# Kernel tuning notes

Measured on AMD Instinct MI355X. Metric: run time of the kernel, lower is better.

Reference implementation:

```python
import jax, jax.numpy as jnp
import numpy as np

N = 100000   # nodes
E = 1600000  # edges
D = 64       # in_features == out_features (residual requires equality)
BN_EPS = 1e-5


def setup_inputs() -> dict:
    key = jax.random.key(0)
    ks = jax.random.split(key, 12)
    s = 1.0 / np.sqrt(D)
    inp = {
        "x": jax.random.normal(ks[0], (N, D), dtype=jnp.float32),
        "edge_index": jax.random.randint(ks[1], (2, E), 0, N, dtype=jnp.int64),
        # ResGatedGraphConv params: key/query/value/skip linears
        "Wk": jax.random.uniform(ks[2], (D, D), jnp.float32, -s, s),
        "bk": jax.random.uniform(ks[3], (D,), jnp.float32, -s, s),
        "Wq": jax.random.uniform(ks[4], (D, D), jnp.float32, -s, s),
        "bq": jax.random.uniform(ks[5], (D,), jnp.float32, -s, s),
        "Wv": jax.random.uniform(ks[6], (D, D), jnp.float32, -s, s),
        "bv": jax.random.uniform(ks[7], (D,), jnp.float32, -s, s),
        "Ws": jax.random.uniform(ks[8], (D, D), jnp.float32, -s, s),
        "bs": jax.random.uniform(ks[9], (D,), jnp.float32, -s, s),
        # BatchNorm1d affine params
        "gamma": jnp.ones((D,), jnp.float32),
        "beta": jnp.zeros((D,), jnp.float32),
    }
    return inp


def reference(x, edge_index, Wk, bk, Wq, bq, Wv, bv, Ws, bs, gamma, beta):
    # PyG ResGatedGraphConv:
    #   out_i = W_s x_i + b_s + sum_{(j->i)} sigmoid(k_i + q_j) * v_j
    # where k = lin_key(x), q = lin_query(x), v = lin_value(x).
    src = edge_index[0]  # source nodes j
    dst = edge_index[1]  # target nodes i

    k = x @ Wk.T + bk  # [N, D]
    q = x @ Wq.T + bq  # [N, D]
    v = x @ Wv.T + bv  # [N, D]

    gate = jax.nn.sigmoid(k[dst] + q[src])        # [E, D]
    msg = gate * v[src]                            # [E, D]
    agg = jax.ops.segment_sum(msg, dst, num_segments=x.shape[0])  # [N, D]

    h = agg + x @ Ws.T + bs

    # BatchNorm1d (training mode: batch statistics, biased variance)
    mean = jnp.mean(h, axis=0)
    var = jnp.var(h, axis=0)
    h = (h - mean) * jax.lax.rsqrt(var + BN_EPS) * gamma + beta

    h = jax.nn.relu(h)
    h = h + x  # residual
    # dropout: identity in eval / deterministic reference
    return h
```

## Files before the change

### kernel.cpp

```cpp
#include <hip/hip_runtime.h>
#include <hip/hip_bf16.h>
#include <math.h>

#define N_NODES 100000
#define N_EDGES 1600000
#define D_FEAT  64
#define BN_EPS  1e-5f

#define NBUCKET 196
#define NBUCKET_PAD 256
#define BUCKET_SHIFT 9
#define NBLK_E  196
#define EPB     8192
#define CCAP    96
#define DCAP    14336
#define GEMM_BLOCKS 1563

typedef __attribute__((ext_vector_type(8))) short bf16x8;
typedef __attribute__((ext_vector_type(4))) float f32x4;

static __device__ __forceinline__ short f2bf(float f) {
    __hip_bfloat16 h = __float2bfloat16(f);
    return __builtin_bit_cast(short, h);
}


__global__ __launch_bounds__(256) void gemm4_scatter_kernel(
    const float* __restrict__ x,
    const float* __restrict__ Wk, const float* __restrict__ bk,
    const float* __restrict__ Wq, const float* __restrict__ bq,
    const float* __restrict__ Wv, const float* __restrict__ bv,
    const float* __restrict__ Ws, const float* __restrict__ bs,
    unsigned char* __restrict__ mix,
    unsigned short* __restrict__ kp,
    float* __restrict__ h0,
    const int* __restrict__ ei,
    int* __restrict__ counts,
    unsigned int* __restrict__ chunks)
{
    __shared__ short xs[64 * 64];
    __shared__ unsigned short kt[64][68];
    __shared__ unsigned short qt[64][68];
    __shared__ unsigned short vt[64][68];
    __shared__ int hcnt[NBUCKET_PAD];

    if (blockIdx.x >= GEMM_BLOCKS) {
        const int cb = blockIdx.x - GEMM_BLOCKS;
        hcnt[threadIdx.x] = 0;
        __syncthreads();
        const int base = cb * EPB;
        for (int i = threadIdx.x; i < EPB; i += 256) {
            const int e = base + i;
            if (e < N_EDGES) {
                const int s = ei[e];
                const int d = ei[N_EDGES + e];
                const int b = d >> BUCKET_SHIFT;
                const int pos = atomicAdd(&hcnt[b], 1);
                if (pos < CCAP)
                    chunks[((size_t)b * NBLK_E + cb) * CCAP + pos] =
                        ((unsigned int)s << BUCKET_SHIFT) | (unsigned int)(d & 511);
            }
        }
        __syncthreads();
        if (threadIdx.x < NBUCKET)
            counts[threadIdx.x * NBLK_E + cb] = min(hcnt[threadIdx.x], CCAP);
        return;
    }

    const int lane = threadIdx.x & 63;
    const int wave = threadIdx.x >> 6;
    const int r0 = blockIdx.x * 64;

    const float* W; const float* b;
    if      (wave == 0) { W = Wk; b = bk; }
    else if (wave == 1) { W = Wq; b = bq; }
    else if (wave == 2) { W = Wv; b = bv; }
    else                { W = Ws; b = bs; }

    const int bcol = lane & 15;
    const int bk0  = (lane >> 4) * 8;
    bf16x8 bfrag[4][2];
    #pragma unroll
    for (int nt = 0; nt < 4; ++nt) {
        #pragma unroll
        for (int ks = 0; ks < 2; ++ks) {
            const float* wp = W + (nt * 16 + bcol) * 64 + ks * 32 + bk0;
            const float4 w0 = *reinterpret_cast<const float4*>(wp);
            const float4 w1 = *reinterpret_cast<const float4*>(wp + 4);
            bf16x8 f;
            f[0] = f2bf(w0.x); f[1] = f2bf(w0.y); f[2] = f2bf(w0.z); f[3] = f2bf(w0.w);
            f[4] = f2bf(w1.x); f[5] = f2bf(w1.y); f[6] = f2bf(w1.z); f[7] = f2bf(w1.w);
            bfrag[nt][ks] = f;
        }
    }
    float biasv[4];
    #pragma unroll
    for (int nt = 0; nt < 4; ++nt) biasv[nt] = b[nt * 16 + bcol];

    {
        const int row = threadIdx.x >> 2;
        const int qd  = threadIdx.x & 3;
        const int grow = r0 + row;
        float4 t0, t1, t2, t3;
        if (grow < N_NODES) {
            const float* xp = x + (size_t)grow * 64 + qd * 16;
            t0 = reinterpret_cast<const float4*>(xp)[0];
            t1 = reinterpret_cast<const float4*>(xp)[1];
            t2 = reinterpret_cast<const float4*>(xp)[2];
            t3 = reinterpret_cast<const float4*>(xp)[3];
        } else {
            t0 = t1 = t2 = t3 = make_float4(0.f, 0.f, 0.f, 0.f);
        }
        bf16x8 u0, u1;
        u0[0] = f2bf(t0.x); u0[1] = f2bf(t0.y); u0[2] = f2bf(t0.z); u0[3] = f2bf(t0.w);
        u0[4] = f2bf(t1.x); u0[5] = f2bf(t1.y); u0[6] = f2bf(t1.z); u0[7] = f2bf(t1.w);
        u1[0] = f2bf(t2.x); u1[1] = f2bf(t2.y); u1[2] = f2bf(t2.z); u1[3] = f2bf(t2.w);
        u1[4] = f2bf(t3.x); u1[5] = f2bf(t3.y); u1[6] = f2bf(t3.z); u1[7] = f2bf(t3.w);
        const int sw = row & 7;
        *reinterpret_cast<bf16x8*>(xs + row * 64 + (((qd * 2)     ^ sw) * 8)) = u0;
        *reinterpret_cast<bf16x8*>(xs + row * 64 + (((qd * 2 + 1) ^ sw) * 8)) = u1;
    }
    __syncthreads();

    f32x4 acc[4][4];
    #pragma unroll
    for (int mt = 0; mt < 4; ++mt)
        #pragma unroll
        for (int nt = 0; nt < 4; ++nt)
            acc[mt][nt] = (f32x4){biasv[nt], biasv[nt], biasv[nt], biasv[nt]};

    const int arow = lane & 15;
    const int ak   = lane >> 4;
    #pragma unroll
    for (int mt = 0; mt < 4; ++mt) {
        const int row = mt * 16 + arow;
        const int sw = row & 7;
        const bf16x8 a0 = *reinterpret_cast<const bf16x8*>(xs + row * 64 + ((ak       ^ sw) * 8));
        const bf16x8 a1 = *reinterpret_cast<const bf16x8*>(xs + row * 64 + (((4 + ak) ^ sw) * 8));
        #pragma unroll
        for (int nt = 0; nt < 4; ++nt) {
            acc[mt][nt] = __builtin_amdgcn_mfma_f32_16x16x32_bf16(
                a0, bfrag[nt][0], acc[mt][nt], 0, 0, 0);
            acc[mt][nt] = __builtin_amdgcn_mfma_f32_16x16x32_bf16(
                a1, bfrag[nt][1], acc[mt][nt], 0, 0, 0);
        }
    }

    const int crow0 = (lane >> 4) * 4;
    const int ccol  = lane & 15;
    if (wave < 3) {
        unsigned short (*tile)[68] = (wave == 0) ? kt : (wave == 1) ? qt : vt;
        #pragma unroll
        for (int mt = 0; mt < 4; ++mt)
            #pragma unroll
            for (int nt = 0; nt < 4; ++nt)
                #pragma unroll
                for (int r = 0; r < 4; ++r)
                    tile[mt * 16 + crow0 + r][nt * 16 + ccol] =
                        (unsigned short)f2bf(acc[mt][nt][r]);
    } else {
        #pragma unroll
        for (int mt = 0; mt < 4; ++mt)
            #pragma unroll
            for (int nt = 0; nt < 4; ++nt)
                #pragma unroll
                for (int r = 0; r < 4; ++r) {
                    const int grow = r0 + mt * 16 + crow0 + r;
                    if (grow < N_NODES)
                        h0[(size_t)grow * 64 + nt * 16 + ccol] = acc[mt][nt][r];
                }
    }
    __syncthreads();

    {
        const int row = threadIdx.x >> 2;
        const int seg = threadIdx.x & 3;
        const int grow = r0 + row;
        if (grow < N_NODES) {
            const int c0 = seg * 16;
            unsigned char* mrow = mix + (size_t)grow * 192;

            unsigned int qd[4];
            #pragma unroll
            for (int i = 0; i < 4; ++i) {
                const float f0 = __uint_as_float((unsigned int)qt[row][c0 + 4*i + 0] << 16);
                const float f1 = __uint_as_float((unsigned int)qt[row][c0 + 4*i + 1] << 16);
                const float f2 = __uint_as_float((unsigned int)qt[row][c0 + 4*i + 2] << 16);
                const float f3 = __uint_as_float((unsigned int)qt[row][c0 + 4*i + 3] << 16);
                int p = __builtin_amdgcn_cvt_pk_fp8_f32(f0, f1, 0, false);
                p = __builtin_amdgcn_cvt_pk_fp8_f32(f2, f3, p, true);
                qd[i] = (unsigned int)p;
            }
            *reinterpret_cast<uint4*>(mrow + c0) =
                make_uint4(qd[0], qd[1], qd[2], qd[3]);

            unsigned int vd[8];
            #pragma unroll
            for (int i = 0; i < 8; ++i)
                vd[i] = (unsigned int)vt[row][c0 + 2 * i] |
                        ((unsigned int)vt[row][c0 + 2 * i + 1] << 16);
            uint4* vdst = reinterpret_cast<uint4*>(mrow + 64 + seg * 32);
            vdst[0] = make_uint4(vd[0], vd[1], vd[2], vd[3]);
            vdst[1] = make_uint4(vd[4], vd[5], vd[6], vd[7]);

            unsigned int kd[8];
            #pragma unroll
            for (int i = 0; i < 8; ++i)
                kd[i] = (unsigned int)kt[row][c0 + 2 * i] |
                        ((unsigned int)kt[row][c0 + 2 * i + 1] << 16);
            uint4* kdst = reinterpret_cast<uint4*>(kp + (size_t)grow * 64 + c0);
            kdst[0] = make_uint4(kd[0], kd[1], kd[2], kd[3]);
            kdst[1] = make_uint4(kd[4], kd[5], kd[6], kd[7]);
        }
    }
}

__global__ __launch_bounds__(512) void bucket_sort_kernel(
    const int* __restrict__ counts,
    unsigned int* __restrict__ chunks,
    int2* __restrict__ row_se)
{
    __shared__ unsigned int stage[DCAP];
    __shared__ int hist[512];
    __shared__ int cursor[512];
    __shared__ int cpre[256];
    const int b = blockIdx.x;
    const int t = threadIdx.x;

    int myc = 0;
    if (t < 256) {
        myc = (t < NBLK_E) ? counts[b * NBLK_E + t] : 0;
        cpre[t] = myc;
    }
    __syncthreads();
    for (int off = 1; off < 256; off <<= 1) {
        int val = 0;
        if (t < 256 && t >= off) val = cpre[t - off];
        __syncthreads();
        if (t < 256) cpre[t] += val;
        __syncthreads();
    }
    const int total = cpre[255];

    if (t < NBLK_E && myc > 0) {
        const int dst0 = cpre[t] - myc;
        const unsigned int* src = chunks + ((size_t)b * NBLK_E + t) * CCAP;
        for (int c = 0; c < myc; ++c) {
            const int d = dst0 + c;
            if (d < DCAP) stage[d] = src[c];
        }
    }
    hist[t] = 0;
    __syncthreads();

    int sz = total;
    if (sz > DCAP) sz = DCAP;
    for (int i = t; i < sz; i += 512) atomicAdd(&hist[stage[i] & 511], 1);
    __syncthreads();
    const int myv = hist[t];
    for (int off = 1; off < 512; off <<= 1) {
        const int u = (t >= off) ? hist[t - off] : 0;
        __syncthreads();
        hist[t] += u;
        __syncthreads();
    }
    const int excl = hist[t] - myv;
    const int node = b * 512 + t;
    const int obase = b * NBLK_E * CCAP;
    if (node < N_NODES)
        row_se[node] = make_int2(obase + excl, obase + excl + myv);
    cursor[t] = excl;
    __syncthreads();

    unsigned int* out = chunks + (size_t)obase;
    for (int i = t; i < sz; i += 512) {
        const unsigned int pk = stage[i];
        const int pos = atomicAdd(&cursor[(int)(pk & 511)], 1);
        out[pos] = pk >> BUCKET_SHIFT;
    }
}

static __device__ __forceinline__ void edge4(
    float4& acc, const float4& kf, unsigned int qb, uint2 vb)
{
    const float q0 = __builtin_amdgcn_cvt_f32_fp8(qb, 0);
    const float q1 = __builtin_amdgcn_cvt_f32_fp8(qb, 1);
    const float q2 = __builtin_amdgcn_cvt_f32_fp8(qb, 2);
    const float q3 = __builtin_amdgcn_cvt_f32_fp8(qb, 3);
    const float v0 = __uint_as_float(vb.x << 16);
    const float v1 = __uint_as_float(vb.x & 0xffff0000u);
    const float v2 = __uint_as_float(vb.y << 16);
    const float v3 = __uint_as_float(vb.y & 0xffff0000u);
    acc.x = fmaf(__builtin_amdgcn_rcpf(1.0f + __expf(-(kf.x + q0))), v0, acc.x);
    acc.y = fmaf(__builtin_amdgcn_rcpf(1.0f + __expf(-(kf.y + q1))), v1, acc.y);
    acc.z = fmaf(__builtin_amdgcn_rcpf(1.0f + __expf(-(kf.z + q2))), v2, acc.z);
    acc.w = fmaf(__builtin_amdgcn_rcpf(1.0f + __expf(-(kf.w + q3))), v3, acc.w);
}

__global__ __launch_bounds__(256, 4) void gather_kernel(
    const unsigned char* __restrict__ mix,
    const unsigned short* __restrict__ kp,
    const int2* __restrict__ row_se,
    const unsigned int* __restrict__ sorted_src,
    float* __restrict__ h0, float* __restrict__ stats)
{
    const int lane = threadIdx.x & 63;
    const int sub  = lane >> 4;
    const int l    = lane & 15;
    const int wave = threadIdx.x >> 6;

    float4 lsum = make_float4(0.f, 0.f, 0.f, 0.f);
    float4 lsq  = make_float4(0.f, 0.f, 0.f, 0.f);

    const int quad0  = blockIdx.x * 4 + wave;
    const int qstride = gridDim.x * 4;
    const int nquads = N_NODES / 4;

    for (int quad = quad0; quad < nquads; quad += qstride) {
        const int n = quad * 4 + sub;
        const int2 se = row_se[n];
        const int base = se.x;
        const int end  = se.y;
        const int deg  = end - base;

        int m1 = max(deg, __shfl_xor(deg, 16));
        const int maxdeg = max(m1, __shfl_xor(m1, 32));

        const ushort4 kr = *reinterpret_cast<const ushort4*>(kp + (size_t)n * 64 + 4 * l);
        float4 kf;
        kf.x = __uint_as_float((unsigned int)kr.x << 16);
        kf.y = __uint_as_float((unsigned int)kr.y << 16);
        kf.z = __uint_as_float((unsigned int)kr.z << 16);
        kf.w = __uint_as_float((unsigned int)kr.w << 16);
        float4 acc = *reinterpret_cast<const float4*>(h0 + (size_t)n * 64 + 4 * l);

        const int safe_last = max(end - 1, 0);

        for (int t = 0; t < maxdeg; t += 4) {
            const int i0 = min(base + t + 0, safe_last);
            const int i1 = min(base + t + 1, safe_last);
            const int i2 = min(base + t + 2, safe_last);
            const int i3 = min(base + t + 3, safe_last);
            const int s0 = min((int)sorted_src[i0], N_NODES - 1);
            const int s1 = min((int)sorted_src[i1], N_NODES - 1);
            const int s2 = min((int)sorted_src[i2], N_NODES - 1);
            const int s3 = min((int)sorted_src[i3], N_NODES - 1);
            const size_t r0 = (size_t)s0 * 192;
            const size_t r1 = (size_t)s1 * 192;
            const size_t r2 = (size_t)s2 * 192;
            const size_t r3 = (size_t)s3 * 192;
            const unsigned int qb0 = *reinterpret_cast<const unsigned int*>(mix + r0 + 4 * l);
            const unsigned int qb1 = *reinterpret_cast<const unsigned int*>(mix + r1 + 4 * l);
            const unsigned int qb2 = *reinterpret_cast<const unsigned int*>(mix + r2 + 4 * l);
            const unsigned int qb3 = *reinterpret_cast<const unsigned int*>(mix + r3 + 4 * l);
            uint2 vb0 = *reinterpret_cast<const uint2*>(mix + r0 + 64 + 8 * l);
            uint2 vb1 = *reinterpret_cast<const uint2*>(mix + r1 + 64 + 8 * l);
            uint2 vb2 = *reinterpret_cast<const uint2*>(mix + r2 + 64 + 8 * l);
            uint2 vb3 = *reinterpret_cast<const uint2*>(mix + r3 + 64 + 8 * l);
            const bool m0 = (t + 0) < deg, m1b = (t + 1) < deg,
                       m2 = (t + 2) < deg, m3 = (t + 3) < deg;
            vb0.x = m0 ? vb0.x : 0u;  vb0.y = m0 ? vb0.y : 0u;
            vb1.x = m1b ? vb1.x : 0u; vb1.y = m1b ? vb1.y : 0u;
            vb2.x = m2 ? vb2.x : 0u;  vb2.y = m2 ? vb2.y : 0u;
            vb3.x = m3 ? vb3.x : 0u;  vb3.y = m3 ? vb3.y : 0u;

            edge4(acc, kf, qb0, vb0);
            edge4(acc, kf, qb1, vb1);
            edge4(acc, kf, qb2, vb2);
            edge4(acc, kf, qb3, vb3);
        }

        *reinterpret_cast<float4*>(h0 + (size_t)n * 64 + 4 * l) = acc;
        lsum.x += acc.x; lsum.y += acc.y; lsum.z += acc.z; lsum.w += acc.w;
        lsq.x += acc.x * acc.x; lsq.y += acc.y * acc.y;
        lsq.z += acc.z * acc.z; lsq.w += acc.w * acc.w;
    }

    __shared__ float bsum[64];
    __shared__ float bsq[64];
    if (threadIdx.x < 64) { bsum[threadIdx.x] = 0.f; bsq[threadIdx.x] = 0.f; }
    __syncthreads();
    atomicAdd(&bsum[4 * l + 0], lsum.x); atomicAdd(&bsq[4 * l + 0], lsq.x);
    atomicAdd(&bsum[4 * l + 1], lsum.y); atomicAdd(&bsq[4 * l + 1], lsq.y);
    atomicAdd(&bsum[4 * l + 2], lsum.z); atomicAdd(&bsq[4 * l + 2], lsq.z);
    atomicAdd(&bsum[4 * l + 3], lsum.w); atomicAdd(&bsq[4 * l + 3], lsq.w);
    __syncthreads();
    if (threadIdx.x < 64) {
        atomicAdd(&stats[threadIdx.x], bsum[threadIdx.x]);
        atomicAdd(&stats[64 + threadIdx.x], bsq[threadIdx.x]);
    }
}

__global__ __launch_bounds__(256) void final_kernel(
    float* __restrict__ h0, const float* __restrict__ x,
    const float* __restrict__ stats,
    const float* __restrict__ gamma, const float* __restrict__ beta)
{
    const int lane = threadIdx.x & 63;
    const int sub  = lane >> 4;
    const int l    = lane & 15;
    const int wave = threadIdx.x >> 6;

    const float invN = 1.0f / (float)N_NODES;
    const float4 s1 = *reinterpret_cast<const float4*>(stats + 4 * l);
    const float4 s2 = *reinterpret_cast<const float4*>(stats + 64 + 4 * l);
    const float4 g  = *reinterpret_cast<const float4*>(gamma + 4 * l);
    const float4 bt = *reinterpret_cast<const float4*>(beta + 4 * l);
    float4 mean, a;
    mean.x = s1.x * invN; mean.y = s1.y * invN;
    mean.z = s1.z * invN; mean.w = s1.w * invN;
    a.x = rsqrtf(s2.x * invN - mean.x * mean.x + BN_EPS) * g.x;
    a.y = rsqrtf(s2.y * invN - mean.y * mean.y + BN_EPS) * g.y;
    a.z = rsqrtf(s2.z * invN - mean.z * mean.z + BN_EPS) * g.z;
    a.w = rsqrtf(s2.w * invN - mean.w * mean.w + BN_EPS) * g.w;

    const int quad0  = blockIdx.x * 4 + wave;
    const int qstride = gridDim.x * 4;
    const int nquads = N_NODES / 4;

    for (int quad = quad0; quad < nquads; quad += qstride) {
        const int n = quad * 4 + sub;
        const size_t off = (size_t)n * 64 + 4 * l;
        const float4 h  = *reinterpret_cast<const float4*>(h0 + off);
        const float4 xx = *reinterpret_cast<const float4*>(x + off);
        float4 y;
        y.x = fmaxf((h.x - mean.x) * a.x + bt.x, 0.f) + xx.x;
        y.y = fmaxf((h.y - mean.y) * a.y + bt.y, 0.f) + xx.y;
        y.z = fmaxf((h.z - mean.z) * a.z + bt.z, 0.f) + xx.z;
        y.w = fmaxf((h.w - mean.w) * a.w + bt.w, 0.f) + xx.w;
        *reinterpret_cast<float4*>(h0 + off) = y;
    }
}

extern "C" void kernel_launch(void* const* d_in, const int* in_sizes, int n_in,
                              void* d_out, int out_size, void* d_ws, size_t ws_size,
                              hipStream_t stream)
{
    const float* x     = (const float*)d_in[0];
    const int*   ei    = (const int*)d_in[1];
    const float* Wk    = (const float*)d_in[2];
    const float* bk    = (const float*)d_in[3];
    const float* Wq    = (const float*)d_in[4];
    const float* bq    = (const float*)d_in[5];
    const float* Wv    = (const float*)d_in[6];
    const float* bv    = (const float*)d_in[7];
    const float* Ws    = (const float*)d_in[8];
    const float* bs    = (const float*)d_in[9];
    const float* gamma = (const float*)d_in[10];
    const float* beta  = (const float*)d_in[11];

    char* w = (char*)d_ws;
    unsigned char*  mix  = (unsigned char*)w;
    unsigned short* kpl  = (unsigned short*)(w + 19200000);
    float* stats      = (float*)(w + 32000000);
    int*   counts     = (int*)  (w + 32000512);
    int2*  row_se     = (int2*) (w + 32154176);
    unsigned int* chunks = (unsigned int*)(w + 32954176);

    float* h0 = (float*)d_out;

    hipMemsetAsync(stats, 0, 512, stream);

    gemm4_scatter_kernel<<<GEMM_BLOCKS + NBLK_E, 256, 0, stream>>>(
        x, Wk, bk, Wq, bq, Wv, bv, Ws, bs, mix, kpl, h0, ei, counts, chunks);

    bucket_sort_kernel<<<NBUCKET, 512, 0, stream>>>(counts, chunks, row_se);

    gather_kernel<<<2084, 256, 0, stream>>>(
        mix, kpl, row_se, chunks, h0, stats);

    final_kernel<<<2084, 256, 0, stream>>>(h0, x, stats, gamma, beta);
}
```

Before: 185.8 us.

## Fuse gather and batchnorm-finalize kernels via grid-wide barrier, keep accumulators in registers

Merges the gather and final BatchNorm/ReLU/residual kernels into one persistent kernel of 1024 blocks. A global atomic counter acts as a grid barrier once the statistics are accumulated, and each thread keeps its up to 7 per-node accumulators in registers. This removes a kernel launch and the write-then-reread of the pre-normalisation h0 buffer. In exchange it relies on all 1024 blocks being co-resident to avoid deadlock, and the extra registers may lower occupancy or latency hiding in the gather loop.

New measurement: 482.4 us. +159.6%, slower.

```diff
diff --git a/kernel.cpp b/kernel.cpp
--- a/kernel.cpp
+++ b/kernel.cpp
@@ -15,6 +15,11 @@
 #define CCAP    96
 #define DCAP    14336
 #define GEMM_BLOCKS 1563
+
+#define GGRID   1024
+#define GWAVES  (GGRID * 4)
+#define NQUADS  (N_NODES / 4)
+#define GITERS  7
 
 typedef __attribute__((ext_vector_type(8))) short bf16x8;
 typedef __attribute__((ext_vector_type(4))) float f32x4;
@@ -297,87 +302,95 @@
     acc.w = fmaf(__builtin_amdgcn_rcpf(1.0f + __expf(-(kf.w + q3))), v3, acc.w);
 }
 
-__global__ __launch_bounds__(256, 4) void gather_kernel(
+__global__ __launch_bounds__(256, 4) void gather_final_kernel(
     const unsigned char* __restrict__ mix,
     const unsigned short* __restrict__ kp,
     const int2* __restrict__ row_se,
     const unsigned int* __restrict__ sorted_src,
-    float* __restrict__ h0, float* __restrict__ stats)
+    float* __restrict__ h0,
+    const float* __restrict__ x,
+    const float* __restrict__ gamma, const float* __restrict__ beta,
+    float* __restrict__ stats, int* __restrict__ counter)
 {
     const int lane = threadIdx.x & 63;
     const int sub  = lane >> 4;
     const int l    = lane & 15;
     const int wave = threadIdx.x >> 6;
+    const int wave_id = blockIdx.x * 4 + wave;
+
+    __shared__ float bsum[64];
+    __shared__ float bsq[64];
+    __shared__ float sstat[128];
 
     float4 lsum = make_float4(0.f, 0.f, 0.f, 0.f);
     float4 lsq  = make_float4(0.f, 0.f, 0.f, 0.f);
-
-    const int quad0  = blockIdx.x * 4 + wave;
-    const int qstride = gridDim.x * 4;
-    const int nquads = N_NODES / 4;
-
-    for (int quad = quad0; quad < nquads; quad += qstride) {
-        const int n = quad * 4 + sub;
-        const int2 se = row_se[n];
-        const int base = se.x;
-        const int end  = se.y;
-        const int deg  = end - base;
-
-        int m1 = max(deg, __shfl_xor(deg, 16));
-        const int maxdeg = max(m1, __shfl_xor(m1, 32));
-
-        const ushort4 kr = *reinterpret_cast<const ushort4*>(kp + (size_t)n * 64 + 4 * l);
-        float4 kf;
-        kf.x = __uint_as_float((unsigned int)kr.x << 16);
-        kf.y = __uint_as_float((unsigned int)kr.y << 16);
-        kf.z = __uint_as_float((unsigned int)kr.z << 16);
-        kf.w = __uint_as_float((unsigned int)kr.w << 16);
-        float4 acc = *reinterpret_cast<const float4*>(h0 + (size_t)n * 64 + 4 * l);
-
-        const int safe_last = max(end - 1, 0);
-
-        for (int t = 0; t < maxdeg; t += 4) {
-            const int i0 = min(base + t + 0, safe_last);
-            const int i1 = min(base + t + 1, safe_last);
-            const int i2 = min(base + t + 2, safe_last);
-            const int i3 = min(base + t + 3, safe_last);
-            const int s0 = min((int)sorted_src[i0], N_NODES - 1);
-            const int s1 = min((int)sorted_src[i1], N_NODES - 1);
-            const int s2 = min((int)sorted_src[i2], N_NODES - 1);
-            const int s3 = min((int)sorted_src[i3], N_NODES - 1);
-            const size_t r0 = (size_t)s0 * 192;
-            const size_t r1 = (size_t)s1 * 192;
-            const size_t r2 = (size_t)s2 * 192;
-            const size_t r3 = (size_t)s3 * 192;
-            const unsigned int qb0 = *reinterpret_cast<const unsigned int*>(mix + r0 + 4 * l);
-            const unsigned int qb1 = *reinterpret_cast<const unsigned int*>(mix + r1 + 4 * l);
-            const unsigned int qb2 = *reinterpret_cast<const unsigned int*>(mix + r2 + 4 * l);
-            const unsigned int qb3 = *reinterpret_cast<const unsigned int*>(mix + r3 + 4 * l);
-            uint2 vb0 = *reinterpret_cast<const uint2*>(mix + r0 + 64 + 8 * l);
-            uint2 vb1 = *reinterpret_cast<const uint2*>(mix + r1 + 64 + 8 * l);
-            uint2 vb2 = *reinterpret_cast<const uint2*>(mix + r2 + 64 + 8 * l);
-            uint2 vb3 = *reinterpret_cast<const uint2*>(mix + r3 + 64 + 8 * l);
-            const bool m0 = (t + 0) < deg, m1b = (t + 1) < deg,
-                       m2 = (t + 2) < deg, m3 = (t + 3) < deg;
-            vb0.x = m0 ? vb0.x : 0u;  vb0.y = m0 ? vb0.y : 0u;
-            vb1.x = m1b ? vb1.x : 0u; vb1.y = m1b ? vb1.y : 0u;
-            vb2.x = m2 ? vb2.x : 0u;  vb2.y = m2 ? vb2.y : 0u;
-            vb3.x = m3 ? vb3.x : 0u;  vb3.y = m3 ? vb3.y : 0u;
-
-            edge4(acc, kf, qb0, vb0);
-            edge4(acc, kf, qb1, vb1);
-            edge4(acc, kf, qb2, vb2);
-            edge4(acc, kf, qb3, vb3);
-        }
-
-        *reinterpret_cast<float4*>(h0 + (size_t)n * 64 + 4 * l) = acc;
-        lsum.x += acc.x; lsum.y += acc.y; lsum.z += acc.z; lsum.w += acc.w;
-        lsq.x += acc.x * acc.x; lsq.y += acc.y * acc.y;
-        lsq.z += acc.z * acc.z; lsq.w += acc.w * acc.w;
-    }
-
-    __shared__ float bsum[64];
-    __shared__ float bsq[64];
+    float4 acc[GITERS];
+
+    #pragma unroll
+    for (int i = 0; i < GITERS; ++i) {
+        acc[i] = make_float4(0.f, 0.f, 0.f, 0.f);
+        const int quad = wave_id + i * GWAVES;
+        if (quad < NQUADS) {
+            const int n = quad * 4 + sub;
+            const int2 se = row_se[n];
+            const int base = se.x;
+            const int end  = se.y;
+            const int deg  = end - base;
+
+            int m1 = max(deg, __shfl_xor(deg, 16));
+            const int maxdeg = max(m1, __shfl_xor(m1, 32));
+
+            const ushort4 kr = *reinterpret_cast<const ushort4*>(kp + (size_t)n * 64 + 4 * l);
+            float4 kf;
+            kf.x = __uint_as_float((unsigned int)kr.x << 16);
+            kf.y = __uint_as_float((unsigned int)kr.y << 16);
+            kf.z = __uint_as_float((unsigned int)kr.z << 16);
+            kf.w = __uint_as_float((unsigned int)kr.w << 16);
+            acc[i] = *reinterpret_cast<const float4*>(h0 + (size_t)n * 64 + 4 * l);
+
+            const int safe_last = max(end - 1, 0);
+
+            for (int t = 0; t < maxdeg; t += 4) {
+                const int i0 = min(base + t + 0, safe_last);
+                const int i1 = min(base + t + 1, safe_last);
+                const int i2 = min(base + t + 2, safe_last);
+                const int i3 = min(base + t + 3, safe_last);
+                const int s0 = min((int)sorted_src[i0], N_NODES - 1);
+                const int s1 = min((int)sorted_src[i1], N_NODES - 1);
+                const int s2 = min((int)sorted_src[i2], N_NODES - 1);
+                const int s3 = min((int)sorted_src[i3], N_NODES - 1);
+                const size_t r0 = (size_t)s0 * 192;
+                const size_t r1 = (size_t)s1 * 192;
+                const size_t r2 = (size_t)s2 * 192;
+                const size_t r3 = (size_t)s3 * 192;
+                const unsigned int qb0 = *reinterpret_cast<const unsigned int*>(mix + r0 + 4 * l);
+                const unsigned int qb1 = *reinterpret_cast<const unsigned int*>(mix + r1 + 4 * l);
+                const unsigned int qb2 = *reinterpret_cast<const unsigned int*>(mix + r2 + 4 * l);
+                const unsigned int qb3 = *reinterpret_cast<const unsigned int*>(mix + r3 + 4 * l);
+                uint2 vb0 = *reinterpret_cast<const uint2*>(mix + r0 + 64 + 8 * l);
+                uint2 vb1 = *reinterpret_cast<const uint2*>(mix + r1 + 64 + 8 * l);
+                uint2 vb2 = *reinterpret_cast<const uint2*>(mix + r2 + 64 + 8 * l);
+                uint2 vb3 = *reinterpret_cast<const uint2*>(mix + r3 + 64 + 8 * l);
+                const bool m0 = (t + 0) < deg, m1b = (t + 1) < deg,
+                           m2 = (t + 2) < deg, m3 = (t + 3) < deg;
+                vb0.x = m0 ? vb0.x : 0u;  vb0.y = m0 ? vb0.y : 0u;
+                vb1.x = m1b ? vb1.x : 0u; vb1.y = m1b ? vb1.y : 0u;
+                vb2.x = m2 ? vb2.x : 0u;  vb2.y = m2 ? vb2.y : 0u;
+                vb3.x = m3 ? vb3.x : 0u;  vb3.y = m3 ? vb3.y : 0u;
+
+                edge4(acc[i], kf, qb0, vb0);
+                edge4(acc[i], kf, qb1, vb1);
+                edge4(acc[i], kf, qb2, vb2);
+                edge4(acc[i], kf, qb3, vb3);
+            }
+
+            lsum.x += acc[i].x; lsum.y += acc[i].y;
+            lsum.z += acc[i].z; lsum.w += acc[i].w;
+            lsq.x += acc[i].x * acc[i].x; lsq.y += acc[i].y * acc[i].y;
+            lsq.z += acc[i].z * acc[i].z; lsq.w += acc[i].w * acc[i].w;
+        }
+    }
+
     if (threadIdx.x < 64) { bsum[threadIdx.x] = 0.f; bsq[threadIdx.x] = 0.f; }
     __syncthreads();
     atomicAdd(&bsum[4 * l + 0], lsum.x); atomicAdd(&bsq[4 * l + 0], lsq.x);
@@ -389,46 +402,49 @@
         atomicAdd(&stats[threadIdx.x], bsum[threadIdx.x]);
         atomicAdd(&stats[64 + threadIdx.x], bsq[threadIdx.x]);
     }
-}
-
-__global__ __launch_bounds__(256) void final_kernel(
-    float* __restrict__ h0, const float* __restrict__ x,
-    const float* __restrict__ stats,
-    const float* __restrict__ gamma, const float* __restrict__ beta)
-{
-    const int lane = threadIdx.x & 63;
-    const int sub  = lane >> 4;
-    const int l    = lane & 15;
-    const int wave = threadIdx.x >> 6;
+
+    __syncthreads();
+    if (threadIdx.x == 0) {
+        __hip_atomic_fetch_add(counter, 1, __ATOMIC_RELEASE,
+                               __HIP_MEMORY_SCOPE_AGENT);
+        while (__hip_atomic_load(counter, __ATOMIC_ACQUIRE,
+                                 __HIP_MEMORY_SCOPE_AGENT) < GGRID) {
+            __builtin_amdgcn_s_sleep(8);
+        }
+    }
+    __syncthreads();
+
+    if (threadIdx.x < 128)
+        sstat[threadIdx.x] = __hip_atomic_load(&stats[threadIdx.x],
+                                               __ATOMIC_RELAXED,
+                                               __HIP_MEMORY_SCOPE_AGENT);
+    __syncthreads();
 
     const float invN = 1.0f / (float)N_NODES;
-    const float4 s1 = *reinterpret_cast<const float4*>(stats + 4 * l);
-    const float4 s2 = *reinterpret_cast<const float4*>(stats + 64 + 4 * l);
     const float4 g  = *reinterpret_cast<const float4*>(gamma + 4 * l);
     const float4 bt = *reinterpret_cast<const float4*>(beta + 4 * l);
     float4 mean, a;
-    mean.x = s1.x * invN; mean.y = s1.y * invN;
-    mean.z = s1.z * invN; mean.w = s1.w * invN;
-    a.x = rsqrtf(s2.x * invN - mean.x * mean.x + BN_EPS) * g.x;
-    a.y = rsqrtf(s2.y * invN - mean.y * mean.y + BN_EPS) * g.y;
-    a.z = rsqrtf(s2.z * invN - mean.z * mean.z + BN_EPS) * g.z;
-    a.w = rsqrtf(s2.w * invN - mean.w * mean.w + BN_EPS) * g.w;
-
-    const int quad0  = blockIdx.x * 4 + wave;
-    const int qstride = gridDim.x * 4;
-    const int nquads = N_NODES / 4;
-
-    for (int quad = quad0; quad < nquads; quad += qstride) {
-        const int n = quad * 4 + sub;
-        const size_t off = (size_t)n * 64 + 4 * l;
-        const float4 h  = *reinterpret_cast<const float4*>(h0 + off);
-        const float4 xx = *reinterpret_cast<const float4*>(x + off);
-        float4 y;
-        y.x = fmaxf((h.x - mean.x) * a.x + bt.x, 0.f) + xx.x;
-        y.y = fmaxf((h.y - mean.y) * a.y + bt.y, 0.f) + xx.y;
-        y.z = fmaxf((h.z - mean.z) * a.z + bt.z, 0.f) + xx.z;
-        y.w = fmaxf((h.w - mean.w) * a.w + bt.w, 0.f) + xx.w;
-        *reinterpret_cast<float4*>(h0 + off) = y;
+    mean.x = sstat[4 * l + 0] * invN; mean.y = sstat[4 * l + 1] * invN;
+    mean.z = sstat[4 * l + 2] * invN; mean.w = sstat[4 * l + 3] * invN;
+    a.x = rsqrtf(sstat[64 + 4 * l + 0] * invN - mean.x * mean.x + BN_EPS) * g.x;
+    a.y = rsqrtf(sstat[64 + 4 * l + 1] * invN - mean.y * mean.y + BN_EPS) * g.y;
+    a.z = rsqrtf(sstat[64 + 4 * l + 2] * invN - mean.z * mean.z + BN_EPS) * g.z;
+    a.w = rsqrtf(sstat[64 + 4 * l + 3] * invN - mean.w * mean.w + BN_EPS) * g.w;
+
+    #pragma unroll
+    for (int i = 0; i < GITERS; ++i) {
+        const int quad = wave_id + i * GWAVES;
+        if (quad < NQUADS) {
+            const int n = quad * 4 + sub;
+            const size_t off = (size_t)n * 64 + 4 * l;
+            const float4 xx = *reinterpret_cast<const float4*>(x + off);
+            float4 y;
+            y.x = fmaxf((acc[i].x - mean.x) * a.x + bt.x, 0.f) + xx.x;
+            y.y = fmaxf((acc[i].y - mean.y) * a.y + bt.y, 0.f) + xx.y;
+            y.z = fmaxf((acc[i].z - mean.z) * a.z + bt.z, 0.f) + xx.z;
+            y.w = fmaxf((acc[i].w - mean.w) * a.w + bt.w, 0.f) + xx.w;
+            *reinterpret_cast<float4*>(h0 + off) = y;
+        }
     }
 }
 
@@ -453,21 +469,20 @@
     unsigned char*  mix  = (unsigned char*)w;
     unsigned short* kpl  = (unsigned short*)(w + 19200000);
     float* stats      = (float*)(w + 32000000);
-    int*   counts     = (int*)  (w + 32000512);
-    int2*  row_se     = (int2*) (w + 32154176);
-    unsigned int* chunks = (unsigned int*)(w + 32954176);
+    int*   counter    = (int*)  (w + 32000512);
+    int*   counts     = (int*)  (w + 32000528);
+    int2*  row_se     = (int2*) (w + 32154192);
+    unsigned int* chunks = (unsigned int*)(w + 32954192);
 
     float* h0 = (float*)d_out;
 
-    hipMemsetAsync(stats, 0, 512, stream);
+    hipMemsetAsync(stats, 0, 528, stream);
 
     gemm4_scatter_kernel<<<GEMM_BLOCKS + NBLK_E, 256, 0, stream>>>(
         x, Wk, bk, Wq, bq, Wv, bv, Ws, bs, mix, kpl, h0, ei, counts, chunks);
 
     bucket_sort_kernel<<<NBUCKET, 512, 0, stream>>>(counts, chunks, row_se);
 
-    gather_kernel<<<2084, 256, 0, stream>>>(
-        mix, kpl, row_se, chunks, h0, stats);
-
-    final_kernel<<<2084, 256, 0, stream>>>(h0, x, stats, gamma, beta);
-}
+    gather_final_kernel<<<GGRID, 256, 0, stream>>>(
+        mix, kpl, row_se, chunks, h0, x, gamma, beta, stats, counter);
+}
```
